# Kernel tuning notes

Measured on AMD Instinct MI355X. Metric: run time of the kernel, lower is better.

The kernel has to match this reference:

```python
import jax, jax.numpy as jnp
import numpy as np

N_NODES = 50000
N_EDGES = 800000
NUM_GRAPHS = 256
BN_EPS = 1e-5


def setup_inputs() -> dict:
    key = jax.random.key(0)
    ks = jax.random.split(key, 16)
    in_dim, hid, out_dim = 64, 128, 1
    s = lambda k, shape, fan: jax.random.normal(k, shape, jnp.float32) / np.sqrt(fan)
    inp = {
        'x': jax.random.normal(ks[0], (N_NODES, in_dim), jnp.float32),
        'edge_index': jax.random.randint(ks[1], (2, N_EDGES), 0, N_NODES, jnp.int64),
        'batch': jnp.sort(jax.random.randint(ks[2], (N_NODES,), 0, NUM_GRAPHS, jnp.int64)),
        # SAGEConv layer 0 (in_dim->hid): Wn aggregated-neighbor weight (with bias), Wr root weight
        'Wn0': s(ks[3], (in_dim, hid), in_dim), 'Wr0': s(ks[4], (in_dim, hid), in_dim), 'b0': jnp.zeros((hid,), jnp.float32),
        'Wn1': s(ks[5], (hid, hid), hid), 'Wr1': s(ks[6], (hid, hid), hid), 'b1': jnp.zeros((hid,), jnp.float32),
        'Wn2': s(ks[7], (hid, hid), hid), 'Wr2': s(ks[8], (hid, hid), hid), 'b2': jnp.zeros((hid,), jnp.float32),
        'gamma': jnp.ones((3, hid), jnp.float32), 'beta': jnp.zeros((3, hid), jnp.float32),
        'fc1_W': s(ks[9], (hid, hid // 2), hid), 'fc1_b': jnp.zeros((hid // 2,), jnp.float32),
        'fc2_W': s(ks[10], (hid // 2, out_dim), hid // 2), 'fc2_b': jnp.zeros((out_dim,), jnp.float32),
    }
    return inp


def _sage_mean(x, src, dst, inv_deg, Wn, Wr, b):
    # mean-aggregate neighbor features then linear: lin_l(mean_j x_j) + lin_r(x_i)
    agg = jax.ops.segment_sum(x[src], dst, num_segments=N_NODES) * inv_deg
    return agg @ Wn + x @ Wr + b


def _bn_relu(h, g, bta):
    mu = jnp.mean(h, axis=0)
    var = jnp.var(h, axis=0)
    return jax.nn.relu((h - mu) * jax.lax.rsqrt(var + BN_EPS) * g + bta)


def reference(x, edge_index, batch, Wn0, Wr0, b0, Wn1, Wr1, b1, Wn2, Wr2, b2,
              gamma, beta, fc1_W, fc1_b, fc2_W, fc2_b):
    src, dst = edge_index[0], edge_index[1]
    deg = jax.ops.segment_sum(jnp.ones((src.shape[0],), x.dtype), dst, num_segments=N_NODES)
    inv_deg = (1.0 / jnp.maximum(deg, 1.0))[:, None]  # [N,1]

    h = _bn_relu(_sage_mean(x, src, dst, inv_deg, Wn0, Wr0, b0), gamma[0], beta[0])
    h = _bn_relu(_sage_mean(h, src, dst, inv_deg, Wn1, Wr1, b1), gamma[1], beta[1])
    h = _bn_relu(_sage_mean(h, src, dst, inv_deg, Wn2, Wr2, b2), gamma[2], beta[2])

    # global mean pool over graphs
    pooled = jax.ops.segment_sum(h, batch, num_segments=NUM_GRAPHS)
    cnt = jax.ops.segment_sum(jnp.ones((h.shape[0],), h.dtype), batch, num_segments=NUM_GRAPHS)
    pooled = pooled / jnp.maximum(cnt, 1.0)[:, None]

    z = jax.nn.relu(pooled @ fc1_W + fc1_b)
    return jax.nn.sigmoid(z @ fc2_W + fc2_b)  # [NUM_GRAPHS, 1]
```

## Files before the change

kernel.cpp:

```cpp
#include <hip/hip_runtime.h>

#define N_NODES 50000
#define N_EDGES 800000
#define NUM_GRAPHS 256
#define HID 128
#define IN_DIM 64
#define BN_EPS 1e-5f
#define SPREAD 64
#define NB 196
#define BUCKET 256
#define SCHUNK 4096

typedef __attribute__((ext_vector_type(8))) short bf16x8;
typedef __attribute__((ext_vector_type(4))) float f32x4;

__device__ __forceinline__ float bf2f(unsigned short u){ union{unsigned i;float f;}c; c.i=((unsigned)u)<<16; return c.f; }
__device__ __forceinline__ float bflo(unsigned w){ union{unsigned i;float f;}c; c.i=w<<16; return c.f; }
__device__ __forceinline__ float bfhi(unsigned w){ union{unsigned i;float f;}c; c.i=w&0xFFFF0000u; return c.f; }
__device__ __forceinline__ unsigned short f2bf(float f){ union{float f;unsigned i;}c; c.f=f; unsigned r=c.i+0x7FFF+((c.i>>16)&1); return (unsigned short)(r>>16); }
__device__ __forceinline__ unsigned fpack(float a, float b){
  union{float f;unsigned i;}ca,cb; ca.f=a; cb.f=b;
  unsigned ra=((ca.i+0x7FFF+((ca.i>>16)&1))>>16)&0xFFFFu;
  unsigned rb=(cb.i+0x7FFF+((cb.i>>16)&1))&0xFFFF0000u;
  return ra|rb;
}

__global__ __launch_bounds__(256) void k_hist(const int* __restrict__ dst, int* __restrict__ bcount){
  __shared__ int h[NB];
  int t = threadIdx.x;
  for(int i=t;i<NB;i+=256) h[i]=0;
  __syncthreads();
  int base = blockIdx.x*SCHUNK;
  int n = min(SCHUNK, N_EDGES-base);
  for(int v=t; v<n; v+=256) atomicAdd(&h[dst[base+v]>>8], 1);
  __syncthreads();
  for(int i=t;i<NB;i+=256) if(h[i]) atomicAdd(&bcount[i], h[i]);
}

__global__ __launch_bounds__(256) void k_bucketscan(const int* __restrict__ bcount, int* __restrict__ bbase,
                                                    int* __restrict__ bfill, int* __restrict__ rowptr){
  __shared__ int sh[256];
  int t = threadIdx.x;
  int v = (t<NB)? bcount[t] : 0;
  sh[t]=v; __syncthreads();
  for(int off=1;off<256;off<<=1){ int u=(t>=off)?sh[t-off]:0; __syncthreads(); sh[t]+=u; __syncthreads(); }
  if(t<NB){ bbase[t]=sh[t]-v; bfill[t]=sh[t]-v; }
  if(t==0){ bbase[NB]=N_EDGES; rowptr[N_NODES]=N_EDGES; }
}

__global__ __launch_bounds__(256) void k_bscatter(const int* __restrict__ src, const int* __restrict__ dst,
                                                  int* __restrict__ bfill, uint2* __restrict__ pairs){
  __shared__ int h[NB], lbase[NB], gbase[NB], cur[NB];
  __shared__ int sc[256];
  __shared__ uint2 staged[SCHUNK];
  int t = threadIdx.x;
  for(int i=t;i<NB;i+=256) h[i]=0;
  __syncthreads();
  int base = blockIdx.x*SCHUNK;
  int n = min(SCHUNK, N_EDGES-base);
  for(int v=t; v<n; v+=256) atomicAdd(&h[dst[base+v]>>8], 1);
  __syncthreads();
  int hv = (t<NB)? h[t] : 0;
  sc[t]=hv; __syncthreads();
  for(int off=1;off<256;off<<=1){ int u=(t>=off)?sc[t-off]:0; __syncthreads(); sc[t]+=u; __syncthreads(); }
  if(t<NB){ lbase[t]=sc[t]-hv; cur[t]=0; if(hv) gbase[t]=atomicAdd(&bfill[t], hv); }
  __syncthreads();
  for(int v=t; v<n; v+=256){
    int s = src[base+v], d = dst[base+v];
    int b = d>>8;
    int r = atomicAdd(&cur[b], 1);
    staged[lbase[b]+r] = make_uint2((unsigned)s,(unsigned)d);
  }
  __syncthreads();
  for(int i=t; i<n; i+=256){
    uint2 p = staged[i];
    int b = (int)(p.y>>8);
    pairs[gbase[b] + (i - lbase[b])] = p;
  }
}

__global__ __launch_bounds__(1024) void k_csr(const uint2* __restrict__ pairs, const int* __restrict__ bbase,
                                              int* __restrict__ rowptr, float* __restrict__ invdeg,
                                              int* __restrict__ eidx){
  __shared__ int cnt[BUCKET], cur[BUCKET], sc[BUCKET];
  int t = threadIdx.x;
  int b = blockIdx.x;
  int node0 = b*BUCKET;
  int nn = min(BUCKET, N_NODES-node0);
  if(t<BUCKET) cnt[t]=0;
  __syncthreads();
  int e0 = bbase[b], e1 = bbase[b+1];
  for(int i=e0+t; i<e1; i+=1024) atomicAdd(&cnt[(int)pairs[i].y - node0], 1);
  __syncthreads();
  if(t<BUCKET) sc[t]=cnt[t];
  __syncthreads();
  for(int off=1;off<BUCKET;off<<=1){
    int u=0;
    if(t<BUCKET && t>=off) u=sc[t-off];
    __syncthreads();
    if(t<BUCKET) sc[t]+=u;
    __syncthreads();
  }
  if(t<nn){
    int pre = sc[t]-cnt[t] + e0;
    rowptr[node0+t] = pre;
    cur[t] = pre;
    invdeg[node0+t] = 1.0f/(float)max(cnt[t],1);
  }
  __syncthreads();
  for(int i=e0+t; i<e1; i+=1024){
    uint2 p = pairs[i];
    int pos = atomicAdd(&cur[(int)p.y - node0], 1);
    eidx[pos] = (int)p.x;
  }
}

__global__ __launch_bounds__(256) void k_packX(const float* __restrict__ x, unsigned short* __restrict__ F0){
  int tid = blockIdx.x*256 + threadIdx.x;
  if(tid >= N_NODES*8) return;
  int row = tid>>3, q = tid&7;
  float4 a = ((const float4*)x)[(size_t)row*16 + q*2];
  float4 b = ((const float4*)x)[(size_t)row*16 + q*2 + 1];
  uint4 o;
  o.x = fpack(a.x, a.y); o.y = fpack(a.z, a.w);
  o.z = fpack(b.x, b.y); o.w = fpack(b.z, b.w);
  ((uint4*)F0)[(size_t)row*16 + 8 + q] = o;
}

template<int KH>
__global__ __launch_bounds__(256) void k_packW(const float* __restrict__ Wn, const float* __restrict__ Wr,
                                               unsigned short* __restrict__ Bp){
  const int NKS = (2*KH)/32;
  int id = blockIdx.x*256 + threadIdx.x;
  if(id >= 8*NKS*64) return;
  int lane = id & 63;
  int ks = (id>>6) % NKS;
  int nt = (id>>6) / NKS;
  int quad = lane>>4, m = lane&15;
  int c = nt*16 + m;
  unsigned short v[8];
  #pragma unroll
  for(int j=0;j<8;j++){
    int k = ks*32 + quad*8 + j;
    float w = (k < KH) ? Wn[(size_t)k*HID + c] : Wr[(size_t)(k-KH)*HID + c];
    v[j] = f2bf(w);
  }
  uint4 o;
  o.x = ((unsigned)v[1]<<16)|v[0]; o.y = ((unsigned)v[3]<<16)|v[2];
  o.z = ((unsigned)v[5]<<16)|v[4]; o.w = ((unsigned)v[7]<<16)|v[6];
  ((uint4*)Bp)[id] = o;
}

template<int KH>
__global__ __launch_bounds__(256) void k_agg(unsigned short* __restrict__ F, const int* __restrict__ eidx,
                      const int* __restrict__ rowptr, const float* __restrict__ invdeg){
  const int F8 = KH/8;
  const int RPI = 64/F8;
  const int KS = 2*KH;
  int wave = threadIdx.x >> 6;
  int lane = threadIdx.x & 63;
  int n = blockIdx.x*4 + wave;
  int b = rowptr[n], e = rowptr[n+1];
  int r = lane / F8, q = lane % F8;
  float acc[8] = {0,0,0,0,0,0,0,0};
  for(int i = b + r; i < e; i += RPI){
    int s = eidx[i];
    uint4 u = *(const uint4*)(F + (size_t)s*KS + KH + q*8);
    acc[0] += bflo(u.x); acc[1] += bfhi(u.x);
    acc[2] += bflo(u.y); acc[3] += bfhi(u.y);
    acc[4] += bflo(u.z); acc[5] += bfhi(u.z);
    acc[6] += bflo(u.w); acc[7] += bfhi(u.w);
  }
  #pragma unroll
  for(int off = F8; off < 64; off <<= 1){
    #pragma unroll
    for(int k=0;k<8;k++) acc[k] += __shfl_xor(acc[k], off, 64);
  }
  if(lane < F8){
    float id = invdeg[n];
    uint4 o;
    o.x = fpack(acc[0]*id, acc[1]*id); o.y = fpack(acc[2]*id, acc[3]*id);
    o.z = fpack(acc[4]*id, acc[5]*id); o.w = fpack(acc[6]*id, acc[7]*id);
    *(uint4*)(F + (size_t)n*KS + q*8) = o;
  }
}

template<int K>
__global__ __launch_bounds__(256) void k_gemm(const unsigned short* __restrict__ F,
                     const unsigned short* __restrict__ Bp, const float* __restrict__ bias,
                     unsigned short* __restrict__ raw,
                     float* __restrict__ psum, float* __restrict__ psq){
  const int NKS = K/32;
  int wave = threadIdx.x>>6, lane = threadIdx.x&63;
  int row0w = blockIdx.x*64 + wave*16;
  if(row0w >= N_NODES) return;
  int m = lane&15, quad = lane>>4;
  const unsigned short* Arow = F + (size_t)(row0w+m)*K + quad*8;
  f32x4 acc[8];
  #pragma unroll
  for(int nt=0;nt<8;nt++) acc[nt] = (f32x4){0.f,0.f,0.f,0.f};
  #pragma unroll 1
  for(int ks=0; ks<NKS; ks++){
    bf16x8 a = *(const bf16x8*)(Arow + ks*32);
    const unsigned short* bp = Bp + ((size_t)ks*64 + lane)*8;
    #pragma unroll
    for(int nt=0;nt<8;nt++){
      bf16x8 b = *(const bf16x8*)(bp + (size_t)nt*NKS*64*8);
      acc[nt] = __builtin_amdgcn_mfma_f32_16x16x32_bf16(a, b, acc[nt], 0, 0, 0);
    }
  }
  int sp = blockIdx.x & (SPREAD-1);
  #pragma unroll
  for(int nt=0;nt<8;nt++){
    int col = nt*16 + m;
    float bv = bias[col];
    float s = 0.f, s2 = 0.f;
    #pragma unroll
    for(int reg=0;reg<4;reg++){
      float v = acc[nt][reg] + bv;
      int row = row0w + quad*4 + reg;
      raw[(size_t)row*HID + col] = f2bf(v);
      s += v; s2 += v*v;
    }
    s  += __shfl_xor(s, 16, 64);  s  += __shfl_xor(s, 32, 64);
    s2 += __shfl_xor(s2, 16, 64); s2 += __shfl_xor(s2, 32, 64);
    if(quad==0){
      atomicAdd(&psum[sp*HID+col], s);
      atomicAdd(&psq [sp*HID+col], s2);
    }
  }
}

__global__ void k_bnfinal(const float* __restrict__ psum, const float* __restrict__ psq,
                          const float* __restrict__ gamma, const float* __restrict__ beta,
                          float* __restrict__ scale, float* __restrict__ shift){
  int t = threadIdx.x;
  float s = 0.f, s2 = 0.f;
  for(int i=0;i<SPREAD;i++){ s += psum[i*HID+t]; s2 += psq[i*HID+t]; }
  float mu  = s  * (1.0f/(float)N_NODES);
  float var = s2 * (1.0f/(float)N_NODES) - mu*mu;
  float rstd = rsqrtf(var + BN_EPS);
  float sc = rstd * gamma[t];
  scale[t] = sc;
  shift[t] = beta[t] - mu*sc;
}

__global__ __launch_bounds__(256) void k_transform(const unsigned short* __restrict__ raw,
                     const float* __restrict__ scale, const float* __restrict__ shift,
                     unsigned short* __restrict__ Fn){
  int tid = blockIdx.x*256 + threadIdx.x;
  if(tid >= N_NODES*16) return;
  int row = tid>>4, q = tid&15;
  uint4 u = ((const uint4*)raw)[(size_t)row*16 + q];
  float4 sc0 = ((const float4*)scale)[q*2], sc1 = ((const float4*)scale)[q*2+1];
  float4 sf0 = ((const float4*)shift)[q*2], sf1 = ((const float4*)shift)[q*2+1];
  float f0 = fmaxf(fmaf(bflo(u.x), sc0.x, sf0.x), 0.f);
  float f1 = fmaxf(fmaf(bfhi(u.x), sc0.y, sf0.y), 0.f);
  float f2 = fmaxf(fmaf(bflo(u.y), sc0.z, sf0.z), 0.f);
  float f3 = fmaxf(fmaf(bfhi(u.y), sc0.w, sf0.w), 0.f);
  float f4 = fmaxf(fmaf(bflo(u.z), sc1.x, sf1.x), 0.f);
  float f5 = fmaxf(fmaf(bfhi(u.z), sc1.y, sf1.y), 0.f);
  float f6 = fmaxf(fmaf(bflo(u.w), sc1.z, sf1.z), 0.f);
  float f7 = fmaxf(fmaf(bfhi(u.w), sc1.w, sf1.w), 0.f);
  uint4 o;
  o.x = fpack(f0,f1); o.y = fpack(f2,f3); o.z = fpack(f4,f5); o.w = fpack(f6,f7);
  ((uint4*)Fn)[(size_t)row*32 + 16 + q] = o;
}

__global__ void k_pool(const unsigned short* __restrict__ raw, const int* __restrict__ batch,
                       const float* __restrict__ scale, const float* __restrict__ shift,
                       float* __restrict__ pooled, float* __restrict__ cnt){
  const int CH = 32;
  int f = threadIdx.x;
  float sc = scale[f], sf = shift[f];
  int n0 = blockIdx.x * CH;
  int nEnd = min(n0+CH, N_NODES);
  float acc = 0.f; int cur = -1; int c = 0;
  for(int n=n0;n<nEnd;n++){
    int b = batch[n];
    if(b != cur){
      if(cur >= 0){
        atomicAdd(&pooled[cur*HID+f], acc);
        if(f==0) atomicAdd(&cnt[cur], (float)c);
      }
      acc = 0.f; c = 0; cur = b;
    }
    float v = bf2f(raw[(size_t)n*HID + f]);
    acc += fmaxf(fmaf(v, sc, sf), 0.f);
    c++;
  }
  if(cur >= 0){
    atomicAdd(&pooled[cur*HID+f], acc);
    if(f==0) atomicAdd(&cnt[cur], (float)c);
  }
}

__global__ void k_mlp(const float* __restrict__ pooled, const float* __restrict__ cnt,
                      const float* __restrict__ fc1W, const float* __restrict__ fc1b,
                      const float* __restrict__ fc2W, const float* __restrict__ fc2b,
                      float* __restrict__ out){
  __shared__ float p[HID];
  int g = blockIdx.x; int t = threadIdx.x;
  float ic = 1.0f / fmaxf(cnt[g], 1.0f);
  p[t]      = pooled[g*HID + t]      * ic;
  p[t + 64] = pooled[g*HID + t + 64] * ic;
  __syncthreads();
  float z = fc1b[t];
  #pragma unroll 4
  for(int k=0;k<HID;k++) z += p[k]*fc1W[k*64 + t];
  z = fmaxf(z, 0.f);
  float v = z * fc2W[t];
  #pragma unroll
  for(int off=32; off>0; off>>=1) v += __shfl_down(v, off, 64);
  if(t==0) out[g] = 1.0f/(1.0f + expf(-(v + fc2b[0])));
}

extern "C" void kernel_launch(void* const* d_in, const int* in_sizes, int n_in,
                              void* d_out, int out_size, void* d_ws, size_t ws_size,
                              hipStream_t stream){
  const float* x    = (const float*)d_in[0];
  const int*   ei   = (const int*)d_in[1];
  const int*   batch= (const int*)d_in[2];
  const float* Wn0=(const float*)d_in[3]; const float* Wr0=(const float*)d_in[4]; const float* b0=(const float*)d_in[5];
  const float* Wn1=(const float*)d_in[6]; const float* Wr1=(const float*)d_in[7]; const float* b1=(const float*)d_in[8];
  const float* Wn2=(const float*)d_in[9]; const float* Wr2=(const float*)d_in[10]; const float* b2=(const float*)d_in[11];
  const float* gamma=(const float*)d_in[12]; const float* beta=(const float*)d_in[13];
  const float* fc1W=(const float*)d_in[14]; const float* fc1b=(const float*)d_in[15];
  const float* fc2W=(const float*)d_in[16]; const float* fc2b=(const float*)d_in[17];
  float* out = (float*)d_out;

  char* ws = (char*)d_ws;
  size_t off = 0;
  auto alloc = [&](size_t bytes)->char*{ char* p = ws + off; off += (bytes + 255) & ~(size_t)255; return p; };

  char* zero0   = ws + off;
  int*   bcount = (int*)alloc((size_t)NB*4);
  float* pstats = (float*)alloc((size_t)3*2*SPREAD*HID*4);
  float* pooled = (float*)alloc(((size_t)NUM_GRAPHS*HID + NUM_GRAPHS)*4);
  float* cnt    = pooled + (size_t)NUM_GRAPHS*HID;
  size_t zbytes = (size_t)((ws + off) - zero0);

  unsigned short* F0  = (unsigned short*)alloc((size_t)N_NODES*128*2);
  unsigned short* F1  = (unsigned short*)alloc((size_t)N_NODES*256*2);
  unsigned short* F2  = (unsigned short*)alloc((size_t)N_NODES*256*2);
  unsigned short* raw = (unsigned short*)alloc((size_t)N_NODES*HID*2);
  unsigned short* Bp0 = (unsigned short*)alloc((size_t)8*4*64*8*2);
  unsigned short* Bp1 = (unsigned short*)alloc((size_t)8*8*64*8*2);
  unsigned short* Bp2 = (unsigned short*)alloc((size_t)8*8*64*8*2);
  float* invdeg = (float*)alloc((size_t)N_NODES*4);
  int* rowptr   = (int*)alloc((size_t)(N_NODES+1)*4);
  int* eidx     = (int*)alloc((size_t)N_EDGES*4);
  uint2* pairs  = (uint2*)alloc((size_t)N_EDGES*8);
  int* bbase    = (int*)alloc((size_t)(NB+1)*4);
  int* bfill    = (int*)alloc((size_t)NB*4);
  float* ss     = (float*)alloc((size_t)3*2*HID*4);

  auto psumL = [&](int l){ return pstats + (size_t)l*2*SPREAD*HID; };
  auto psqL  = [&](int l){ return pstats + (size_t)l*2*SPREAD*HID + (size_t)SPREAD*HID; };
  auto scaleL= [&](int l){ return ss + (size_t)l*2*HID; };
  auto shiftL= [&](int l){ return ss + (size_t)l*2*HID + HID; };

  const int* src = ei;
  const int* dst = ei + N_EDGES;

  hipMemsetAsync(zero0, 0, zbytes, stream);

  const int NCHUNK = (N_EDGES + SCHUNK - 1)/SCHUNK;
  k_hist<<<NCHUNK, 256, 0, stream>>>(dst, bcount);
  k_bucketscan<<<1, 256, 0, stream>>>(bcount, bbase, bfill, rowptr);
  k_bscatter<<<NCHUNK, 256, 0, stream>>>(src, dst, bfill, pairs);
  k_csr<<<NB, 1024, 0, stream>>>(pairs, bbase, rowptr, invdeg, eidx);

  k_packX<<<(N_NODES*8+255)/256, 256, 0, stream>>>(x, F0);
  k_packW<IN_DIM><<<(8*4*64+255)/256, 256, 0, stream>>>(Wn0, Wr0, Bp0);
  k_packW<HID><<<(8*8*64+255)/256, 256, 0, stream>>>(Wn1, Wr1, Bp1);
  k_packW<HID><<<(8*8*64+255)/256, 256, 0, stream>>>(Wn2, Wr2, Bp2);

  const int GEMM_BLKS = (N_NODES + 63)/64;

  k_agg<IN_DIM><<<N_NODES/4, 256, 0, stream>>>(F0, eidx, rowptr, invdeg);
  k_gemm<128><<<GEMM_BLKS, 256, 0, stream>>>(F0, Bp0, b0, raw, psumL(0), psqL(0));
  k_bnfinal<<<1, 128, 0, stream>>>(psumL(0), psqL(0), gamma+0*HID, beta+0*HID, scaleL(0), shiftL(0));
  k_transform<<<(N_NODES*16+255)/256, 256, 0, stream>>>(raw, scaleL(0), shiftL(0), F1);

  k_agg<HID><<<N_NODES/4, 256, 0, stream>>>(F1, eidx, rowptr, invdeg);
  k_gemm<256><<<GEMM_BLKS, 256, 0, stream>>>(F1, Bp1, b1, raw, psumL(1), psqL(1));
  k_bnfinal<<<1, 128, 0, stream>>>(psumL(1), psqL(1), gamma+1*HID, beta+1*HID, scaleL(1), shiftL(1));
  k_transform<<<(N_NODES*16+255)/256, 256, 0, stream>>>(raw, scaleL(1), shiftL(1), F2);

  k_agg<HID><<<N_NODES/4, 256, 0, stream>>>(F2, eidx, rowptr, invdeg);
  k_gemm<256><<<GEMM_BLKS, 256, 0, stream>>>(F2, Bp2, b2, raw, psumL(2), psqL(2));
  k_bnfinal<<<1, 128, 0, stream>>>(psumL(2), psqL(2), gamma+2*HID, beta+2*HID, scaleL(2), shiftL(2));

  k_pool<<<(N_NODES+31)/32, 128, 0, stream>>>(raw, batch, scaleL(2), shiftL(2), pooled, cnt);
  k_mlp<<<NUM_GRAPHS, 64, 0, stream>>>(pooled, cnt, fc1W, fc1b, fc2W, fc2b, out);
}
```

Before: 329.9 us.

## Fuse neighbor aggregation into GEMM via LDS and merge prep kernels

Aggregation now runs inside the GEMM kernel. Each block averages neighbor features for its 64 rows into shared memory, then feeds those rows and the root features straight into the MFMA loop, so the aggregated half of the feature buffer is never written to or read back from global memory. Histogram, x packing and weight packing are merged into one launch. The bucket scan and the BN-finalize kernels are folded into their consumers, and SPREAD drops from 64 to 16. This cuts launch count and global traffic, but each block now holds 64 rows of aggregation work before its GEMM and repeats some redundant scans.

```diff
diff --git a/kernel.cpp b/kernel.cpp
--- a/kernel.cpp
+++ b/kernel.cpp
@@ -6,10 +6,14 @@
 #define HID 128
 #define IN_DIM 64
 #define BN_EPS 1e-5f
-#define SPREAD 64
+#define SPREAD 16
 #define NB 196
 #define BUCKET 256
 #define SCHUNK 4096
+#define NCHUNK 196
+#define PX_BLKS 1563
+#define W0_BLKS 8
+#define W1_BLKS 16
 
 typedef __attribute__((ext_vector_type(8))) short bf16x8;
 typedef __attribute__((ext_vector_type(4))) float f32x4;
@@ -25,31 +29,62 @@
   return ra|rb;
 }
 
-__global__ __launch_bounds__(256) void k_hist(const int* __restrict__ dst, int* __restrict__ bcount){
+__global__ __launch_bounds__(256) void k_prep(const int* __restrict__ dst, int* __restrict__ bcount,
+      const float* __restrict__ x, unsigned short* __restrict__ H0,
+      const float* __restrict__ Wn0, const float* __restrict__ Wr0, unsigned short* __restrict__ Bp0,
+      const float* __restrict__ Wn1, const float* __restrict__ Wr1, unsigned short* __restrict__ Bp1,
+      const float* __restrict__ Wn2, const float* __restrict__ Wr2, unsigned short* __restrict__ Bp2){
   __shared__ int h[NB];
-  int t = threadIdx.x;
-  for(int i=t;i<NB;i+=256) h[i]=0;
-  __syncthreads();
-  int base = blockIdx.x*SCHUNK;
-  int n = min(SCHUNK, N_EDGES-base);
-  for(int v=t; v<n; v+=256) atomicAdd(&h[dst[base+v]>>8], 1);
-  __syncthreads();
-  for(int i=t;i<NB;i+=256) if(h[i]) atomicAdd(&bcount[i], h[i]);
-}
-
-__global__ __launch_bounds__(256) void k_bucketscan(const int* __restrict__ bcount, int* __restrict__ bbase,
-                                                    int* __restrict__ bfill, int* __restrict__ rowptr){
-  __shared__ int sh[256];
-  int t = threadIdx.x;
-  int v = (t<NB)? bcount[t] : 0;
-  sh[t]=v; __syncthreads();
-  for(int off=1;off<256;off<<=1){ int u=(t>=off)?sh[t-off]:0; __syncthreads(); sh[t]+=u; __syncthreads(); }
-  if(t<NB){ bbase[t]=sh[t]-v; bfill[t]=sh[t]-v; }
-  if(t==0){ bbase[NB]=N_EDGES; rowptr[N_NODES]=N_EDGES; }
+  int blk = blockIdx.x, t = threadIdx.x;
+  if(blk < NCHUNK){
+    for(int i=t;i<NB;i+=256) h[i]=0;
+    __syncthreads();
+    int base = blk*SCHUNK;
+    int n = min(SCHUNK, N_EDGES-base);
+    for(int v=t; v<n; v+=256) atomicAdd(&h[dst[base+v]>>8], 1);
+    __syncthreads();
+    for(int i=t;i<NB;i+=256) if(h[i]) atomicAdd(&bcount[i], h[i]);
+  } else if(blk < NCHUNK+PX_BLKS){
+    int tid = (blk-NCHUNK)*256 + t;
+    if(tid < N_NODES*8){
+      int row = tid>>3, q = tid&7;
+      float4 a = ((const float4*)x)[(size_t)row*16 + q*2];
+      float4 b = ((const float4*)x)[(size_t)row*16 + q*2 + 1];
+      uint4 o;
+      o.x = fpack(a.x,a.y); o.y = fpack(a.z,a.w);
+      o.z = fpack(b.x,b.y); o.w = fpack(b.z,b.w);
+      ((uint4*)H0)[(size_t)row*8 + q] = o;
+    }
+  } else {
+    const float *Wn, *Wr; unsigned short* Bp; int KH, base;
+    if(blk < NCHUNK+PX_BLKS+W0_BLKS){ Wn=Wn0; Wr=Wr0; Bp=Bp0; KH=IN_DIM; base=NCHUNK+PX_BLKS; }
+    else if(blk < NCHUNK+PX_BLKS+W0_BLKS+W1_BLKS){ Wn=Wn1; Wr=Wr1; Bp=Bp1; KH=HID; base=NCHUNK+PX_BLKS+W0_BLKS; }
+    else { Wn=Wn2; Wr=Wr2; Bp=Bp2; KH=HID; base=NCHUNK+PX_BLKS+W0_BLKS+W1_BLKS; }
+    int NKS = (2*KH)/32;
+    int id = (blk-base)*256 + t;
+    if(id < 8*NKS*64){
+      int lane = id & 63;
+      int ks = (id>>6) % NKS;
+      int nt = (id>>6) / NKS;
+      int quad = lane>>4, m = lane&15;
+      int c = nt*16 + m;
+      unsigned short v[8];
+      #pragma unroll
+      for(int j=0;j<8;j++){
+        int k = ks*32 + quad*8 + j;
+        float w = (k < KH) ? Wn[(size_t)k*HID + c] : Wr[(size_t)(k-KH)*HID + c];
+        v[j] = f2bf(w);
+      }
+      uint4 o;
+      o.x = ((unsigned)v[1]<<16)|v[0]; o.y = ((unsigned)v[3]<<16)|v[2];
+      o.z = ((unsigned)v[5]<<16)|v[4]; o.w = ((unsigned)v[7]<<16)|v[6];
+      ((uint4*)Bp)[id] = o;
+    }
+  }
 }
 
 __global__ __launch_bounds__(256) void k_bscatter(const int* __restrict__ src, const int* __restrict__ dst,
-                                                  int* __restrict__ bfill, uint2* __restrict__ pairs){
+                 const int* __restrict__ bcount, int* __restrict__ bfill, uint2* __restrict__ pairs){
   __shared__ int h[NB], lbase[NB], gbase[NB], cur[NB];
   __shared__ int sc[256];
   __shared__ uint2 staged[SCHUNK];
@@ -60,16 +95,21 @@
   int n = min(SCHUNK, N_EDGES-base);
   for(int v=t; v<n; v+=256) atomicAdd(&h[dst[base+v]>>8], 1);
   __syncthreads();
+  int bc = (t<NB)? bcount[t] : 0;
+  sc[t]=bc; __syncthreads();
+  for(int off=1;off<256;off<<=1){ int u=(t>=off)?sc[t-off]:0; __syncthreads(); sc[t]+=u; __syncthreads(); }
+  int bb_t = sc[t]-bc;
+  __syncthreads();
   int hv = (t<NB)? h[t] : 0;
   sc[t]=hv; __syncthreads();
   for(int off=1;off<256;off<<=1){ int u=(t>=off)?sc[t-off]:0; __syncthreads(); sc[t]+=u; __syncthreads(); }
-  if(t<NB){ lbase[t]=sc[t]-hv; cur[t]=0; if(hv) gbase[t]=atomicAdd(&bfill[t], hv); }
+  if(t<NB){ lbase[t]=sc[t]-hv; cur[t]=0; if(hv) gbase[t] = bb_t + atomicAdd(&bfill[t], hv); }
   __syncthreads();
   for(int v=t; v<n; v+=256){
     int s = src[base+v], d = dst[base+v];
     int b = d>>8;
-    int r = atomicAdd(&cur[b], 1);
-    staged[lbase[b]+r] = make_uint2((unsigned)s,(unsigned)d);
+    int rr = atomicAdd(&cur[b], 1);
+    staged[lbase[b]+rr] = make_uint2((unsigned)s,(unsigned)d);
   }
   __syncthreads();
   for(int i=t; i<n; i+=256){
@@ -79,17 +119,23 @@
   }
 }
 
-__global__ __launch_bounds__(1024) void k_csr(const uint2* __restrict__ pairs, const int* __restrict__ bbase,
-                                              int* __restrict__ rowptr, float* __restrict__ invdeg,
-                                              int* __restrict__ eidx){
+__global__ __launch_bounds__(1024) void k_csr(const uint2* __restrict__ pairs, const int* __restrict__ bcount,
+                int* __restrict__ rowptr, float* __restrict__ invdeg, int* __restrict__ eidx){
   __shared__ int cnt[BUCKET], cur[BUCKET], sc[BUCKET];
+  __shared__ int bb[2];
   int t = threadIdx.x;
   int b = blockIdx.x;
+  if(t==0){ bb[0]=0; bb[1]=0; }
+  if(t<BUCKET) cnt[t]=0;
+  __syncthreads();
+  if(t<NB){
+    int c = bcount[t];
+    if(t<b)  atomicAdd(&bb[0], c);
+    if(t<=b) atomicAdd(&bb[1], c);
+  }
+  __syncthreads();
+  int e0 = bb[0], e1 = bb[1];
   int node0 = b*BUCKET;
-  int nn = min(BUCKET, N_NODES-node0);
-  if(t<BUCKET) cnt[t]=0;
-  __syncthreads();
-  int e0 = bbase[b], e1 = bbase[b+1];
   for(int i=e0+t; i<e1; i+=1024) atomicAdd(&cnt[(int)pairs[i].y - node0], 1);
   __syncthreads();
   if(t<BUCKET) sc[t]=cnt[t];
@@ -101,12 +147,13 @@
     if(t<BUCKET) sc[t]+=u;
     __syncthreads();
   }
-  if(t<nn){
+  if(t<BUCKET && node0+t < N_NODES){
     int pre = sc[t]-cnt[t] + e0;
     rowptr[node0+t] = pre;
     cur[t] = pre;
     invdeg[node0+t] = 1.0f/(float)max(cnt[t],1);
   }
+  if(b==0 && t==0) rowptr[N_NODES] = N_EDGES;
   __syncthreads();
   for(int i=e0+t; i<e1; i+=1024){
     uint2 p = pairs[i];
@@ -115,93 +162,65 @@
   }
 }
 
-__global__ __launch_bounds__(256) void k_packX(const float* __restrict__ x, unsigned short* __restrict__ F0){
-  int tid = blockIdx.x*256 + threadIdx.x;
-  if(tid >= N_NODES*8) return;
-  int row = tid>>3, q = tid&7;
-  float4 a = ((const float4*)x)[(size_t)row*16 + q*2];
-  float4 b = ((const float4*)x)[(size_t)row*16 + q*2 + 1];
-  uint4 o;
-  o.x = fpack(a.x, a.y); o.y = fpack(a.z, a.w);
-  o.z = fpack(b.x, b.y); o.w = fpack(b.z, b.w);
-  ((uint4*)F0)[(size_t)row*16 + 8 + q] = o;
-}
-
 template<int KH>
-__global__ __launch_bounds__(256) void k_packW(const float* __restrict__ Wn, const float* __restrict__ Wr,
-                                               unsigned short* __restrict__ Bp){
-  const int NKS = (2*KH)/32;
-  int id = blockIdx.x*256 + threadIdx.x;
-  if(id >= 8*NKS*64) return;
-  int lane = id & 63;
-  int ks = (id>>6) % NKS;
-  int nt = (id>>6) / NKS;
-  int quad = lane>>4, m = lane&15;
-  int c = nt*16 + m;
-  unsigned short v[8];
-  #pragma unroll
-  for(int j=0;j<8;j++){
-    int k = ks*32 + quad*8 + j;
-    float w = (k < KH) ? Wn[(size_t)k*HID + c] : Wr[(size_t)(k-KH)*HID + c];
-    v[j] = f2bf(w);
-  }
-  uint4 o;
-  o.x = ((unsigned)v[1]<<16)|v[0]; o.y = ((unsigned)v[3]<<16)|v[2];
-  o.z = ((unsigned)v[5]<<16)|v[4]; o.w = ((unsigned)v[7]<<16)|v[6];
-  ((uint4*)Bp)[id] = o;
-}
-
-template<int KH>
-__global__ __launch_bounds__(256) void k_agg(unsigned short* __restrict__ F, const int* __restrict__ eidx,
-                      const int* __restrict__ rowptr, const float* __restrict__ invdeg){
-  const int F8 = KH/8;
-  const int RPI = 64/F8;
-  const int KS = 2*KH;
-  int wave = threadIdx.x >> 6;
-  int lane = threadIdx.x & 63;
-  int n = blockIdx.x*4 + wave;
-  int b = rowptr[n], e = rowptr[n+1];
+__global__ __launch_bounds__(256) void k_agg_gemm(
+    const unsigned short* __restrict__ H,
+    const int* __restrict__ eidx, const int* __restrict__ rowptr, const float* __restrict__ invdeg,
+    const unsigned short* __restrict__ Bp, const float* __restrict__ bias,
+    unsigned short* __restrict__ raw, float* __restrict__ psum, float* __restrict__ psq){
+  const int NKS  = (2*KH)/32;
+  const int LKS  = KH/32;
+  const int F8   = KH/8;
+  const int RPI  = 64/F8;
+  const int ROWU = KH + 8;
+  __shared__ unsigned short aggL[64*ROWU];
+
+  int wave = threadIdx.x>>6, lane = threadIdx.x&63;
+  int n0 = blockIdx.x*64;
   int r = lane / F8, q = lane % F8;
-  float acc[8] = {0,0,0,0,0,0,0,0};
-  for(int i = b + r; i < e; i += RPI){
-    int s = eidx[i];
-    uint4 u = *(const uint4*)(F + (size_t)s*KS + KH + q*8);
-    acc[0] += bflo(u.x); acc[1] += bfhi(u.x);
-    acc[2] += bflo(u.y); acc[3] += bfhi(u.y);
-    acc[4] += bflo(u.z); acc[5] += bfhi(u.z);
-    acc[6] += bflo(u.w); acc[7] += bfhi(u.w);
-  }
-  #pragma unroll
-  for(int off = F8; off < 64; off <<= 1){
-    #pragma unroll
-    for(int k=0;k<8;k++) acc[k] += __shfl_xor(acc[k], off, 64);
-  }
-  if(lane < F8){
-    float id = invdeg[n];
-    uint4 o;
-    o.x = fpack(acc[0]*id, acc[1]*id); o.y = fpack(acc[2]*id, acc[3]*id);
-    o.z = fpack(acc[4]*id, acc[5]*id); o.w = fpack(acc[6]*id, acc[7]*id);
-    *(uint4*)(F + (size_t)n*KS + q*8) = o;
-  }
-}
-
-template<int K>
-__global__ __launch_bounds__(256) void k_gemm(const unsigned short* __restrict__ F,
-                     const unsigned short* __restrict__ Bp, const float* __restrict__ bias,
-                     unsigned short* __restrict__ raw,
-                     float* __restrict__ psum, float* __restrict__ psq){
-  const int NKS = K/32;
-  int wave = threadIdx.x>>6, lane = threadIdx.x&63;
-  int row0w = blockIdx.x*64 + wave*16;
+
+  #pragma unroll 1
+  for(int i=0;i<16;i++){
+    int n = n0 + wave*16 + i;
+    if(n < N_NODES){
+      int b = rowptr[n], e = rowptr[n+1];
+      float acc[8] = {0,0,0,0,0,0,0,0};
+      for(int j=b+r; j<e; j+=RPI){
+        int s = eidx[j];
+        uint4 u = *(const uint4*)(H + (size_t)s*KH + q*8);
+        acc[0]+=bflo(u.x); acc[1]+=bfhi(u.x);
+        acc[2]+=bflo(u.y); acc[3]+=bfhi(u.y);
+        acc[4]+=bflo(u.z); acc[5]+=bfhi(u.z);
+        acc[6]+=bflo(u.w); acc[7]+=bfhi(u.w);
+      }
+      #pragma unroll
+      for(int off=F8; off<64; off<<=1){
+        #pragma unroll
+        for(int k=0;k<8;k++) acc[k] += __shfl_xor(acc[k], off, 64);
+      }
+      if(lane < F8){
+        float id = invdeg[n];
+        uint4 o;
+        o.x = fpack(acc[0]*id, acc[1]*id); o.y = fpack(acc[2]*id, acc[3]*id);
+        o.z = fpack(acc[4]*id, acc[5]*id); o.w = fpack(acc[6]*id, acc[7]*id);
+        *(uint4*)(&aggL[(wave*16+i)*ROWU + q*8]) = o;
+      }
+    }
+  }
+  __syncthreads();
+
+  int row0w = n0 + wave*16;
   if(row0w >= N_NODES) return;
   int m = lane&15, quad = lane>>4;
-  const unsigned short* Arow = F + (size_t)(row0w+m)*K + quad*8;
+  const unsigned short* Hrow = H + (size_t)(row0w+m)*KH + quad*8;
+  const unsigned short* Lrow = &aggL[(wave*16+m)*ROWU + quad*8];
   f32x4 acc[8];
   #pragma unroll
   for(int nt=0;nt<8;nt++) acc[nt] = (f32x4){0.f,0.f,0.f,0.f};
   #pragma unroll 1
   for(int ks=0; ks<NKS; ks++){
-    bf16x8 a = *(const bf16x8*)(Arow + ks*32);
+    bf16x8 a = (ks < LKS) ? *(const bf16x8*)(Lrow + ks*32)
+                          : *(const bf16x8*)(Hrow + (size_t)(ks-LKS)*32);
     const unsigned short* bp = Bp + ((size_t)ks*64 + lane)*8;
     #pragma unroll
     for(int nt=0;nt<8;nt++){
@@ -231,67 +250,73 @@
   }
 }
 
-__global__ void k_bnfinal(const float* __restrict__ psum, const float* __restrict__ psq,
-                          const float* __restrict__ gamma, const float* __restrict__ beta,
-                          float* __restrict__ scale, float* __restrict__ shift){
+__global__ __launch_bounds__(256) void k_transform(const unsigned short* __restrict__ raw,
+      const float* __restrict__ psum, const float* __restrict__ psq,
+      const float* __restrict__ gamma, const float* __restrict__ beta,
+      unsigned short* __restrict__ Hout){
+  __shared__ float s_sc[HID], s_sf[HID];
   int t = threadIdx.x;
-  float s = 0.f, s2 = 0.f;
-  for(int i=0;i<SPREAD;i++){ s += psum[i*HID+t]; s2 += psq[i*HID+t]; }
+  if(t < HID){
+    float s=0.f, s2=0.f;
+    #pragma unroll
+    for(int i=0;i<SPREAD;i++){ s += psum[i*HID+t]; s2 += psq[i*HID+t]; }
+    float mu  = s  * (1.0f/(float)N_NODES);
+    float var = s2 * (1.0f/(float)N_NODES) - mu*mu;
+    float rstd = rsqrtf(var + BN_EPS);
+    float sc = rstd * gamma[t];
+    s_sc[t] = sc; s_sf[t] = beta[t] - mu*sc;
+  }
+  __syncthreads();
+  int tid = blockIdx.x*256 + t;
+  if(tid >= N_NODES*16) return;
+  int q = tid & 15;
+  uint4 u = ((const uint4*)raw)[tid];
+  float f0 = fmaxf(fmaf(bflo(u.x), s_sc[q*8+0], s_sf[q*8+0]), 0.f);
+  float f1 = fmaxf(fmaf(bfhi(u.x), s_sc[q*8+1], s_sf[q*8+1]), 0.f);
+  float f2 = fmaxf(fmaf(bflo(u.y), s_sc[q*8+2], s_sf[q*8+2]), 0.f);
+  float f3 = fmaxf(fmaf(bfhi(u.y), s_sc[q*8+3], s_sf[q*8+3]), 0.f);
+  float f4 = fmaxf(fmaf(bflo(u.z), s_sc[q*8+4], s_sf[q*8+4]), 0.f);
+  float f5 = fmaxf(fmaf(bfhi(u.z), s_sc[q*8+5], s_sf[q*8+5]), 0.f);
+  float f6 = fmaxf(fmaf(bflo(u.w), s_sc[q*8+6], s_sf[q*8+6]), 0.f);
+  float f7 = fmaxf(fmaf(bfhi(u.w), s_sc[q*8+7], s_sf[q*8+7]), 0.f);
+  uint4 o;
+  o.x = fpack(f0,f1); o.y = fpack(f2,f3); o.z = fpack(f4,f5); o.w = fpack(f6,f7);
+  ((uint4*)Hout)[tid] = o;
+}
+
+__global__ __launch_bounds__(128) void k_pool(const unsigned short* __restrict__ raw, const int* __restrict__ batch,
+                       const float* __restrict__ psum, const float* __restrict__ psq,
+                       const float* __restrict__ gamma, const float* __restrict__ beta,
+                       float* __restrict__ pooled, float* __restrict__ cnt){
+  const int CH = 32;
+  int f = threadIdx.x;
+  float s=0.f, s2=0.f;
+  #pragma unroll
+  for(int i=0;i<SPREAD;i++){ s += psum[i*HID+f]; s2 += psq[i*HID+f]; }
   float mu  = s  * (1.0f/(float)N_NODES);
   float var = s2 * (1.0f/(float)N_NODES) - mu*mu;
   float rstd = rsqrtf(var + BN_EPS);
-  float sc = rstd * gamma[t];
-  scale[t] = sc;
-  shift[t] = beta[t] - mu*sc;
-}
-
-__global__ __launch_bounds__(256) void k_transform(const unsigned short* __restrict__ raw,
-                     const float* __restrict__ scale, const float* __restrict__ shift,
-                     unsigned short* __restrict__ Fn){
-  int tid = blockIdx.x*256 + threadIdx.x;
-  if(tid >= N_NODES*16) return;
-  int row = tid>>4, q = tid&15;
-  uint4 u = ((const uint4*)raw)[(size_t)row*16 + q];
-  float4 sc0 = ((const float4*)scale)[q*2], sc1 = ((const float4*)scale)[q*2+1];
-  float4 sf0 = ((const float4*)shift)[q*2], sf1 = ((const float4*)shift)[q*2+1];
-  float f0 = fmaxf(fmaf(bflo(u.x), sc0.x, sf0.x), 0.f);
-  float f1 = fmaxf(fmaf(bfhi(u.x), sc0.y, sf0.y), 0.f);
-  float f2 = fmaxf(fmaf(bflo(u.y), sc0.z, sf0.z), 0.f);
-  float f3 = fmaxf(fmaf(bfhi(u.y), sc0.w, sf0.w), 0.f);
-  float f4 = fmaxf(fmaf(bflo(u.z), sc1.x, sf1.x), 0.f);
-  float f5 = fmaxf(fmaf(bfhi(u.z), sc1.y, sf1.y), 0.f);
-  float f6 = fmaxf(fmaf(bflo(u.w), sc1.z, sf1.z), 0.f);
-  float f7 = fmaxf(fmaf(bfhi(u.w), sc1.w, sf1.w), 0.f);
-  uint4 o;
-  o.x = fpack(f0,f1); o.y = fpack(f2,f3); o.z = fpack(f4,f5); o.w = fpack(f6,f7);
-  ((uint4*)Fn)[(size_t)row*32 + 16 + q] = o;
-}
-
-__global__ void k_pool(const unsigned short* __restrict__ raw, const int* __restrict__ batch,
-                       const float* __restrict__ scale, const float* __restrict__ shift,
-                       float* __restrict__ pooled, float* __restrict__ cnt){
-  const int CH = 32;
-  int f = threadIdx.x;
-  float sc = scale[f], sf = shift[f];
+  float sc = rstd * gamma[f];
+  float sf = beta[f] - mu*sc;
   int n0 = blockIdx.x * CH;
   int nEnd = min(n0+CH, N_NODES);
-  float acc = 0.f; int cur = -1; int c = 0;
+  float acc = 0.f; int curg = -1; int c = 0;
   for(int n=n0;n<nEnd;n++){
     int b = batch[n];
-    if(b != cur){
-      if(cur >= 0){
-        atomicAdd(&pooled[cur*HID+f], acc);
-        if(f==0) atomicAdd(&cnt[cur], (float)c);
+    if(b != curg){
+      if(curg >= 0){
+        atomicAdd(&pooled[curg*HID+f], acc);
+        if(f==0) atomicAdd(&cnt[curg], (float)c);
       }
-      acc = 0.f; c = 0; cur = b;
+      acc = 0.f; c = 0; curg = b;
     }
     float v = bf2f(raw[(size_t)n*HID + f]);
     acc += fmaxf(fmaf(v, sc, sf), 0.f);
     c++;
   }
-  if(cur >= 0){
-    atomicAdd(&pooled[cur*HID+f], acc);
-    if(f==0) atomicAdd(&cnt[cur], (float)c);
+  if(curg >= 0){
+    atomicAdd(&pooled[curg*HID+f], acc);
+    if(f==0) atomicAdd(&cnt[curg], (float)c);
   }
 }
 
@@ -335,14 +360,15 @@
 
   char* zero0   = ws + off;
   int*   bcount = (int*)alloc((size_t)NB*4);
+  int*   bfill  = (int*)alloc((size_t)NB*4);
   float* pstats = (float*)alloc((size_t)3*2*SPREAD*HID*4);
   float* pooled = (float*)alloc(((size_t)NUM_GRAPHS*HID + NUM_GRAPHS)*4);
   float* cnt    = pooled + (size_t)NUM_GRAPHS*HID;
   size_t zbytes = (size_t)((ws + off) - zero0);
 
-  unsigned short* F0  = (unsigned short*)alloc((size_t)N_NODES*128*2);
-  unsigned short* F1  = (unsigned short*)alloc((size_t)N_NODES*256*2);
-  unsigned short* F2  = (unsigned short*)alloc((size_t)N_NODES*256*2);
+  unsigned short* H0  = (unsigned short*)alloc((size_t)N_NODES*IN_DIM*2);
+  unsigned short* H1  = (unsigned short*)alloc((size_t)N_NODES*HID*2);
+  unsigned short* H2  = (unsigned short*)alloc((size_t)N_NODES*HID*2);
   unsigned short* raw = (unsigned short*)alloc((size_t)N_NODES*HID*2);
   unsigned short* Bp0 = (unsigned short*)alloc((size_t)8*4*64*8*2);
   unsigned short* Bp1 = (unsigned short*)alloc((size_t)8*8*64*8*2);
@@ -351,47 +377,28 @@
   int* rowptr   = (int*)alloc((size_t)(N_NODES+1)*4);
   int* eidx     = (int*)alloc((size_t)N_EDGES*4);
   uint2* pairs  = (uint2*)alloc((size_t)N_EDGES*8);
-  int* bbase    = (int*)alloc((size_t)(NB+1)*4);
-  int* bfill    = (int*)alloc((size_t)NB*4);
-  float* ss     = (float*)alloc((size_t)3*2*HID*4);
 
   auto psumL = [&](int l){ return pstats + (size_t)l*2*SPREAD*HID; };
   auto psqL  = [&](int l){ return pstats + (size_t)l*2*SPREAD*HID + (size_t)SPREAD*HID; };
-  auto scaleL= [&](int l){ return ss + (size_t)l*2*HID; };
-  auto shiftL= [&](int l){ return ss + (size_t)l*2*HID + HID; };
 
   const int* src = ei;
   const int* dst = ei + N_EDGES;
 
   hipMemsetAsync(zero0, 0, zbytes, stream);
 
-  const int NCHUNK = (N_EDGES + SCHUNK - 1)/SCHUNK;
-  k_hist<<<NCHUNK, 256, 0, stream>>>(dst, bcount);
-  k_bucketscan<<<1, 256, 0, stream>>>(bcount, bbase, bfill, rowptr);
-  k_bscatter<<<NCHUNK, 256, 0, stream>>>(src, dst, bfill, pairs);
-  k_csr<<<NB, 1024, 0, stream>>>(pairs, bbase, rowptr, invdeg, eidx);
-
-  k_packX<<<(N_NODES*8+255)/256, 256, 0, stream>>>(x, F0);
-  k_packW<IN_DIM><<<(8*4*64+255)/256, 256, 0, stream>>>(Wn0, Wr0, Bp0);
-  k_packW<HID><<<(8*8*64+255)/256, 256, 0, stream>>>(Wn1, Wr1, Bp1);
-  k_packW<HID><<<(8*8*64+255)/256, 256, 0, stream>>>(Wn2, Wr2, Bp2);
+  k_prep<<<NCHUNK+PX_BLKS+W0_BLKS+2*W1_BLKS, 256, 0, stream>>>(dst, bcount, x, H0,
+      Wn0, Wr0, Bp0, Wn1, Wr1, Bp1, Wn2, Wr2, Bp2);
+  k_bscatter<<<NCHUNK, 256, 0, stream>>>(src, dst, bcount, bfill, pairs);
+  k_csr<<<NB, 1024, 0, stream>>>(pairs, bcount, rowptr, invdeg, eidx);
 
   const int GEMM_BLKS = (N_NODES + 63)/64;
 
-  k_agg<IN_DIM><<<N_NODES/4, 256, 0, stream>>>(F0, eidx, rowptr, invdeg);
-  k_gemm<128><<<GEMM_BLKS, 256, 0, stream>>>(F0, Bp0, b0, raw, psumL(0), psqL(0));
-  k_bnfinal<<<1, 128, 0, stream>>>(psumL(0), psqL(0), gamma+0*HID, beta+0*HID, scaleL(0), shiftL(0));
-  k_transform<<<(N_NODES*16+255)/256, 256, 0, stream>>>(raw, scaleL(0), shiftL(0), F1);
-
-  k_agg<HID><<<N_NODES/4, 256, 0, stream>>>(F1, eidx, rowptr, invdeg);
-  k_gemm<256><<<GEMM_BLKS, 256, 0, stream>>>(F1, Bp1, b1, raw, psumL(1), psqL(1));
-  k_bnfinal<<<1, 128, 0, stream>>>(psumL(1), psqL(1), gamma+1*HID, beta+1*HID, scaleL(1), shiftL(1));
-  k_transform<<<(N_NODES*16+255)/256, 256, 0, stream>>>(raw, scaleL(1), shiftL(1), F2);
-
-  k_agg<HID><<<N_NODES/4, 256, 0, stream>>>(F2, eidx, rowptr, invdeg);
-  k_gemm<256><<<GEMM_BLKS, 256, 0, stream>>>(F2, Bp2, b2, raw, psumL(2), psqL(2));
-  k_bnfinal<<<1, 128, 0, stream>>>(psumL(2), psqL(2), gamma+2*HID, beta+2*HID, scaleL(2), shiftL(2));
-
-  k_pool<<<(N_NODES+31)/32, 128, 0, stream>>>(raw, batch, scaleL(2), shiftL(2), pooled, cnt);
+  k_agg_gemm<IN_DIM><<<GEMM_BLKS, 256, 0, stream>>>(H0, eidx, rowptr, invdeg, Bp0, b0, raw, psumL(0), psqL(0));
+  k_transform<<<(N_NODES*16)/256, 256, 0, stream>>>(raw, psumL(0), psqL(0), gamma+0*HID, beta+0*HID, H1);
+  k_agg_gemm<HID><<<GEMM_BLKS, 256, 0, stream>>>(H1, eidx, rowptr, invdeg, Bp1, b1, raw, psumL(1), psqL(1));
+  k_transform<<<(N_NODES*16)/256, 256, 0, stream>>>(raw, psumL(1), psqL(1), gamma+1*HID, beta+1*HID, H2);
+  k_agg_gemm<HID><<<GEMM_BLKS, 256, 0, stream>>>(H2, eidx, rowptr, invdeg, Bp2, b2, raw, psumL(2), psqL(2));
+
+  k_pool<<<(N_NODES+31)/32, 128, 0, stream>>>(raw, batch, psumL(2), psqL(2), gamma+2*HID, beta+2*HID, pooled, cnt);
   k_mlp<<<NUM_GRAPHS, 64, 0, stream>>>(pooled, cnt, fc1W, fc1b, fc2W, fc2b, out);
 }
```

Measured after the change: 376.4 us. 1.14x slower.
